# Kernel optimization log

Measured on AMD Instinct MI355X. Metric: run time of the kernel, lower is better.

The kernel has to match this reference:

```python
import jax, jax.numpy as jnp
import numpy as np

NMS_RADIUS = 0.05  # matches init_kwargs nms_radius


def setup_inputs() -> dict:
    key = jax.random.key(0)
    heatmap = jax.random.normal(key, (64, 1, 1024, 1024), dtype=jnp.float32)
    return {"heatmap": heatmap, "num_candidates": 16}


def _nms_select(coords, num_keep, radius):
    """Greedy sequential 2D NMS over score-sorted coords [k,2].
    torch.topk already returns values sorted descending, so the torch
    argsort(descending=True) is the identity permutation here."""
    k = coords.shape[0]
    # pairwise euclidean distances [k,k]
    d = jnp.linalg.norm(coords[:, None, :] - coords[None, :, :], axis=-1)

    def body(carry, i):
        mask, count = carry  # mask[j] = candidate j already selected
        too_close = jnp.any((d[i] < radius) & mask)
        accept = jnp.logical_and(~too_close, count < num_keep)
        mask = mask.at[i].set(accept)
        count = count + accept.astype(jnp.int32)
        return (mask, count), None

    (mask, _), _ = jax.lax.scan(body, (jnp.zeros(k, bool), jnp.int32(0)), jnp.arange(k))
    # compact: place selected coords (in score order) into the first num_keep slots
    pos = jnp.cumsum(mask) - 1               # output slot for each selected candidate
    slot = jnp.where(mask, pos, num_keep)    # out-of-range slot for unselected -> dropped
    out = jnp.zeros((num_keep, 2), coords.dtype).at[slot].set(coords, mode="drop")
    return out


def reference(heatmap, num_candidates):
    B, _, H, W = heatmap.shape
    flat = heatmap.reshape(B, H * W)
    k = min(num_candidates * 4, H * W)
    top_vals, top_idx = jax.lax.top_k(flat, k)   # sorted descending, like torch.topk
    ty = top_idx // W
    tx = top_idx % W
    # normalized (x, y) in [0,1], shape [B, k, 2]
    coords = jnp.stack([tx.astype(jnp.float32) / (W - 1),
                        ty.astype(jnp.float32) / (H - 1)], axis=-1)
    return jax.vmap(lambda c: _nms_select(c, num_candidates, NMS_RADIUS))(coords)
```

## Files before the change

### kernel.cpp

```cpp
#include <hip/hip_runtime.h>

#define RADIUS 0.05f
#define TH     3.0f
#define SBUF   256
#define SORTN  2048
#define TOPC   128

typedef unsigned long long u64;

__device__ __forceinline__ unsigned fkey(float f) {
  unsigned u = __float_as_uint(f);
  return (u & 0x80000000u) ? ~u : (u | 0x80000000u);
}

__global__ __launch_bounds__(256) void scan_collect(
    const float* __restrict__ hm, unsigned* __restrict__ cnt,
    u64* __restrict__ buf, int bcapblk, int elems, int chunk) {
  const int b   = blockIdx.y;
  const int g   = blockIdx.x;
  const int tid = threadIdx.x;
  const int vbase = g * chunk;
  const float4* p = (const float4*)(hm + (size_t)b * elems) + vbase;

  __shared__ u64 sbuf[SBUF];
  __shared__ unsigned sh;
  if (tid == 0) sh = 0u;
  __syncthreads();

  auto push = [&](float v, int idx) {
    if (v > TH) {
      unsigned pos = atomicAdd(&sh, 1u);
      if (pos < SBUF)
        sbuf[pos] = ((u64)(__float_as_uint(v) | 0x80000000u) << 32) | (unsigned)(~idx);
    }
  };

  int chunkMain = chunk & ~1023;
  for (int i = tid; i < chunkMain; i += 1024) {
    float4 v0 = p[i], v1 = p[i + 256], v2 = p[i + 512], v3 = p[i + 768];
    int g0 = (vbase + i) << 2, g1 = (vbase + i + 256) << 2;
    int g2 = (vbase + i + 512) << 2, g3 = (vbase + i + 768) << 2;
    push(v0.x, g0); push(v0.y, g0 + 1); push(v0.z, g0 + 2); push(v0.w, g0 + 3);
    push(v1.x, g1); push(v1.y, g1 + 1); push(v1.z, g1 + 2); push(v1.w, g1 + 3);
    push(v2.x, g2); push(v2.y, g2 + 1); push(v2.z, g2 + 2); push(v2.w, g2 + 3);
    push(v3.x, g3); push(v3.y, g3 + 1); push(v3.z, g3 + 2); push(v3.w, g3 + 3);
  }
  for (int i = chunkMain + tid; i < chunk; i += 256) {
    float4 v = p[i];
    int gg = (vbase + i) << 2;
    push(v.x, gg); push(v.y, gg + 1); push(v.z, gg + 2); push(v.w, gg + 3);
  }

  __syncthreads();
  unsigned h = sh;
  unsigned cap = (unsigned)bcapblk; if (cap > (unsigned)SBUF) cap = SBUF;
  unsigned stored = h < cap ? h : cap;
  u64* dst = buf + (size_t)(b * 16 + g) * (size_t)bcapblk;
  for (unsigned i = tid; i < stored; i += 256) dst[i] = sbuf[i];
  if (tid == 0)
    cnt[b * 16 + g] = stored | (h > stored ? 0x80000000u : 0u);
}

__global__ __launch_bounds__(256) void select_k(
    const float* __restrict__ hm, const unsigned* __restrict__ cnt,
    const u64* __restrict__ buf, int bcapblk,
    float* __restrict__ out, int W, int H, int K, int nk, int elems) {
  const int b = blockIdx.x, tid = threadIdx.x;

  __shared__ u64 s[SORTN];
  __shared__ unsigned skey[SORTN];
  __shared__ u64 top[TOPC];
  __shared__ unsigned segoff[17];
  __shared__ int s_good, s_m;
  __shared__ unsigned s_cnt;
  __shared__ float topx[64], topy[64];
  __shared__ float outbuf[128];

  if (tid == 0) {
    unsigned tot = 0; int ok = (bcapblk > 0);
    for (int g = 0; g < 16; g++) {
      unsigned cv = (bcapblk > 0) ? cnt[b * 16 + g] : 0u;
      segoff[g] = tot;
      if (cv & 0x80000000u) ok = 0;
      tot += (cv & 0x7FFFFFFFu);
    }
    segoff[16] = tot;
    s_good = ok && tot >= (unsigned)K && tot <= (unsigned)SORTN;
    s_m = 0;
  }
  __syncthreads();
  const int good = s_good;
  const unsigned c = segoff[16];

  if (good) {
    for (int g = 0; g < 16; g++) {
      unsigned off = segoff[g], len = segoff[g + 1] - off;
      const u64* src = buf + (size_t)(b * 16 + g) * (size_t)bcapblk;
      for (unsigned i = tid; i < len; i += 256) {
        u64 e = src[i];
        s[off + i] = e;
        skey[off + i] = (unsigned)(e >> 32);
      }
    }
    __syncthreads();

    unsigned lo = 0xC0400000u;
    unsigned hi = 0xFFFFFFFFu;
    while (lo < hi) {
      unsigned mid = lo + ((hi - lo) >> 1) + 1u;
      if (tid == 0) s_cnt = 0u;
      __syncthreads();
      unsigned local = 0;
      for (unsigned i = tid; i < c; i += 256) local += (skey[i] >= mid);
      #pragma unroll
      for (int o = 32; o > 0; o >>= 1) local += __shfl_xor(local, o);
      if ((tid & 63) == 0) atomicAdd(&s_cnt, local);
      __syncthreads();
      unsigned tot = s_cnt;
      if (tot >= (unsigned)K) lo = mid; else hi = mid - 1u;
      __syncthreads();
    }

    for (unsigned i = tid; i < c; i += 256) {
      if (skey[i] >= lo) {
        int p = atomicAdd(&s_m, 1);
        if (p < TOPC) top[p] = s[i];
      }
    }
    __syncthreads();
  } else {
    unsigned lo = 0u, hi = 0xFFFFFFFFu;
    const float4* p4 = (const float4*)(hm + (size_t)b * elems);
    const int nvec4 = elems >> 2;
    while (lo < hi) {
      unsigned mid = lo + ((hi - lo) >> 1) + 1u;
      if (tid == 0) s_cnt = 0u;
      __syncthreads();
      unsigned local = 0;
      for (int i = tid; i < nvec4; i += 256) {
        float4 v = p4[i];
        local += (fkey(v.x) >= mid) + (fkey(v.y) >= mid) + (fkey(v.z) >= mid) + (fkey(v.w) >= mid);
      }
      #pragma unroll
      for (int o = 32; o > 0; o >>= 1) local += __shfl_xor(local, o);
      if ((tid & 63) == 0) atomicAdd(&s_cnt, local);
      __syncthreads();
      if (s_cnt >= (unsigned)K) lo = mid; else hi = mid - 1u;
      __syncthreads();
    }
    const float* q = hm + (size_t)b * elems;
    for (int i = tid; i < elems; i += 256) {
      unsigned kk = fkey(q[i]);
      if (kk >= lo) {
        int p = atomicAdd(&s_m, 1);
        if (p < TOPC) top[p] = ((u64)kk << 32) | (unsigned)(~i);
      }
    }
    __syncthreads();
  }

  int m = s_m; if (m > TOPC) m = TOPC;
  for (int i = tid; i < TOPC; i += 256) if (i >= m) top[i] = 0ull;
  __syncthreads();
  for (int k2 = 2; k2 <= TOPC; k2 <<= 1) {
    for (int j = k2 >> 1; j > 0; j >>= 1) {
      if (tid < TOPC) {
        int ix = tid ^ j;
        if (ix > tid) {
          u64 a = top[tid], bb = top[ix];
          bool desc = ((tid & k2) == 0);
          if (desc ? (a < bb) : (a > bb)) { top[tid] = bb; top[ix] = a; }
        }
      }
      __syncthreads();
    }
  }

  const float invW = 1.0f / (float)(W - 1);
  const float invH = 1.0f / (float)(H - 1);
  if (tid < K) {
    u64 e = top[tid];
    int idx = (int)(~(unsigned)(e & 0xFFFFFFFFu));
    int ty = idx / W;
    int tx = idx - ty * W;
    topx[tid] = (float)tx * invW;
    topy[tid] = (float)ty * invH;
  }
  for (int i = tid; i < 2 * nk; i += 256) outbuf[i] = 0.0f;
  __syncthreads();

  if (tid < 64) {
    float myx = (tid < K) ? topx[tid] : 0.0f;
    float myy = (tid < K) ? topy[tid] : 0.0f;
    bool sel = false;
    int cntA = 0;
    for (int i = 0; i < K; i++) {
      float xi = __shfl(myx, i);
      float yi = __shfl(myy, i);
      float dx = myx - xi, dy = myy - yi;
      bool close = sel && (sqrtf(dx * dx + dy * dy) < RADIUS);
      u64 anym = __ballot(close);
      bool accept = (anym == 0ull) && (cntA < nk);
      if (tid == i) sel = accept;
      cntA += accept ? 1 : 0;
    }
    u64 selball = __ballot(sel);
    if (sel) {
      int slot = __popcll(selball & ((1ull << tid) - 1ull));
      if (slot < nk) { outbuf[2 * slot] = myx; outbuf[2 * slot + 1] = myy; }
    }
  }
  __syncthreads();

  float* outp = out + (size_t)b * 2 * nk;
  for (int i = tid; i < 2 * nk; i += 256) outp[i] = outbuf[i];
}

extern "C" void kernel_launch(void* const* d_in, const int* in_sizes, int n_in,
                              void* d_out, int out_size, void* d_ws, size_t ws_size,
                              hipStream_t stream) {
  const float* hm = (const float*)d_in[0];
  const int H = 1024, W = 1024;
  const int elems = H * W;
  int B = in_sizes[0] / elems;
  int nk = out_size / (B * 2);
  int K = 4 * nk;
  if (K > elems) K = elems;
  if (K > 64) K = 64;

  unsigned* cnt = (unsigned*)d_ws;
  size_t off_buf = ((size_t)B * 16 * sizeof(unsigned) + 255) & ~(size_t)255;
  u64* buf = (u64*)((char*)d_ws + off_buf);
  int bcapblk = 0;
  if (ws_size > off_buf) {
    size_t avail = ws_size - off_buf;
    long long capl = (long long)(avail / ((size_t)B * 16 * sizeof(u64)));
    bcapblk = (capl > SBUF) ? SBUF : (int)capl;
    if (bcapblk < 16) bcapblk = 0;
  }

  if (bcapblk > 0) {
    const int gx = 16;
    int chunk = (elems >> 2) / gx;
    dim3 grid(gx, B);
    scan_collect<<<grid, 256, 0, stream>>>(hm, cnt, buf, bcapblk, elems, chunk);
  }
  select_k<<<B, 256, 0, stream>>>(hm, cnt, buf, bcapblk, (float*)d_out, W, H, K, nk, elems);
}
```

Before: 400.3 us.

## Deepen nontemporal streaming loads and trim barriers in threshold search

The scan kernel now issues eight nontemporal 16-byte loads per thread per iteration instead of four regular ones, raising memory-level parallelism and bypassing cache retention for the streamed heatmap. The selection kernel splits the packed candidates into separate key and index arrays, bounds the binary search by the actual min/max key, and uses double-buffered accumulators with running bases so each search step needs one barrier instead of three. The risk is extra register pressure in the scan loop. The dominant cost is likely the bandwidth-bound scan, so gains may be small.

```diff
diff --git a/kernel.cpp b/kernel.cpp
--- a/kernel.cpp
+++ b/kernel.cpp
@@ -7,6 +7,7 @@
 #define TOPC   128
 
 typedef unsigned long long u64;
+typedef float __attribute__((ext_vector_type(4))) f4;
 
 __device__ __forceinline__ unsigned fkey(float f) {
   unsigned u = __float_as_uint(f);
@@ -20,7 +21,7 @@
   const int g   = blockIdx.x;
   const int tid = threadIdx.x;
   const int vbase = g * chunk;
-  const float4* p = (const float4*)(hm + (size_t)b * elems) + vbase;
+  const f4* p = (const f4*)(hm + (size_t)b * elems) + vbase;
 
   __shared__ u64 sbuf[SBUF];
   __shared__ unsigned sh;
@@ -35,18 +36,28 @@
     }
   };
 
-  int chunkMain = chunk & ~1023;
-  for (int i = tid; i < chunkMain; i += 1024) {
-    float4 v0 = p[i], v1 = p[i + 256], v2 = p[i + 512], v3 = p[i + 768];
-    int g0 = (vbase + i) << 2, g1 = (vbase + i + 256) << 2;
-    int g2 = (vbase + i + 512) << 2, g3 = (vbase + i + 768) << 2;
-    push(v0.x, g0); push(v0.y, g0 + 1); push(v0.z, g0 + 2); push(v0.w, g0 + 3);
-    push(v1.x, g1); push(v1.y, g1 + 1); push(v1.z, g1 + 2); push(v1.w, g1 + 3);
-    push(v2.x, g2); push(v2.y, g2 + 1); push(v2.z, g2 + 2); push(v2.w, g2 + 3);
-    push(v3.x, g3); push(v3.y, g3 + 1); push(v3.z, g3 + 2); push(v3.w, g3 + 3);
+  int chunkMain = chunk & ~2047;
+  for (int i = tid; i < chunkMain; i += 2048) {
+    f4 v0 = __builtin_nontemporal_load(p + i);
+    f4 v1 = __builtin_nontemporal_load(p + i + 256);
+    f4 v2 = __builtin_nontemporal_load(p + i + 512);
+    f4 v3 = __builtin_nontemporal_load(p + i + 768);
+    f4 v4 = __builtin_nontemporal_load(p + i + 1024);
+    f4 v5 = __builtin_nontemporal_load(p + i + 1280);
+    f4 v6 = __builtin_nontemporal_load(p + i + 1536);
+    f4 v7 = __builtin_nontemporal_load(p + i + 1792);
+    int g0 = (vbase + i) << 2;
+    push(v0.x, g0);        push(v0.y, g0 + 1);    push(v0.z, g0 + 2);    push(v0.w, g0 + 3);
+    push(v1.x, g0 + 1024); push(v1.y, g0 + 1025); push(v1.z, g0 + 1026); push(v1.w, g0 + 1027);
+    push(v2.x, g0 + 2048); push(v2.y, g0 + 2049); push(v2.z, g0 + 2050); push(v2.w, g0 + 2051);
+    push(v3.x, g0 + 3072); push(v3.y, g0 + 3073); push(v3.z, g0 + 3074); push(v3.w, g0 + 3075);
+    push(v4.x, g0 + 4096); push(v4.y, g0 + 4097); push(v4.z, g0 + 4098); push(v4.w, g0 + 4099);
+    push(v5.x, g0 + 5120); push(v5.y, g0 + 5121); push(v5.z, g0 + 5122); push(v5.w, g0 + 5123);
+    push(v6.x, g0 + 6144); push(v6.y, g0 + 6145); push(v6.z, g0 + 6146); push(v6.w, g0 + 6147);
+    push(v7.x, g0 + 7168); push(v7.y, g0 + 7169); push(v7.z, g0 + 7170); push(v7.w, g0 + 7171);
   }
   for (int i = chunkMain + tid; i < chunk; i += 256) {
-    float4 v = p[i];
+    f4 v = __builtin_nontemporal_load(p + i);
     int gg = (vbase + i) << 2;
     push(v.x, gg); push(v.y, gg + 1); push(v.z, gg + 2); push(v.w, gg + 3);
   }
@@ -67,11 +78,13 @@
     float* __restrict__ out, int W, int H, int K, int nk, int elems) {
   const int b = blockIdx.x, tid = threadIdx.x;
 
-  __shared__ u64 s[SORTN];
   __shared__ unsigned skey[SORTN];
+  __shared__ unsigned sidx[SORTN];
   __shared__ u64 top[TOPC];
   __shared__ unsigned segoff[17];
   __shared__ int s_good, s_m;
+  __shared__ unsigned s_acc[2];
+  __shared__ unsigned s_kmin, s_kmax;
   __shared__ unsigned s_cnt;
   __shared__ float topx[64], topy[64];
   __shared__ float outbuf[128];
@@ -87,44 +100,57 @@
     segoff[16] = tot;
     s_good = ok && tot >= (unsigned)K && tot <= (unsigned)SORTN;
     s_m = 0;
+    s_acc[0] = 0u; s_acc[1] = 0u;
+    s_kmin = 0xFFFFFFFFu; s_kmax = 0u;
   }
   __syncthreads();
   const int good = s_good;
   const unsigned c = segoff[16];
 
   if (good) {
+    unsigned lkmin = 0xFFFFFFFFu, lkmax = 0u;
     for (int g = 0; g < 16; g++) {
       unsigned off = segoff[g], len = segoff[g + 1] - off;
       const u64* src = buf + (size_t)(b * 16 + g) * (size_t)bcapblk;
       for (unsigned i = tid; i < len; i += 256) {
         u64 e = src[i];
-        s[off + i] = e;
-        skey[off + i] = (unsigned)(e >> 32);
-      }
-    }
+        unsigned k32 = (unsigned)(e >> 32);
+        skey[off + i] = k32;
+        sidx[off + i] = (unsigned)(e & 0xFFFFFFFFu);
+        lkmin = lkmin < k32 ? lkmin : k32;
+        lkmax = lkmax > k32 ? lkmax : k32;
+      }
+    }
+    #pragma unroll
+    for (int o = 32; o > 0; o >>= 1) {
+      unsigned a = __shfl_xor(lkmin, o); lkmin = lkmin < a ? lkmin : a;
+      unsigned bx = __shfl_xor(lkmax, o); lkmax = lkmax > bx ? lkmax : bx;
+    }
+    if ((tid & 63) == 0) { atomicMin(&s_kmin, lkmin); atomicMax(&s_kmax, lkmax); }
     __syncthreads();
 
-    unsigned lo = 0xC0400000u;
-    unsigned hi = 0xFFFFFFFFu;
+    unsigned lo = s_kmin, hi = s_kmax;
+    unsigned base0 = 0u, base1 = 0u;
+    int it = 0;
     while (lo < hi) {
       unsigned mid = lo + ((hi - lo) >> 1) + 1u;
-      if (tid == 0) s_cnt = 0u;
-      __syncthreads();
       unsigned local = 0;
       for (unsigned i = tid; i < c; i += 256) local += (skey[i] >= mid);
       #pragma unroll
       for (int o = 32; o > 0; o >>= 1) local += __shfl_xor(local, o);
-      if ((tid & 63) == 0) atomicAdd(&s_cnt, local);
-      __syncthreads();
-      unsigned tot = s_cnt;
+      if ((tid & 63) == 0) atomicAdd(&s_acc[it & 1], local);
+      __syncthreads();
+      unsigned acc = s_acc[it & 1];
+      unsigned tot = acc - ((it & 1) ? base1 : base0);
+      if (it & 1) base1 = acc; else base0 = acc;
       if (tot >= (unsigned)K) lo = mid; else hi = mid - 1u;
-      __syncthreads();
+      it++;
     }
 
     for (unsigned i = tid; i < c; i += 256) {
       if (skey[i] >= lo) {
         int p = atomicAdd(&s_m, 1);
-        if (p < TOPC) top[p] = s[i];
+        if (p < TOPC) top[p] = ((u64)skey[i] << 32) | sidx[i];
       }
     }
     __syncthreads();
```

After: 370.5 us. 7.4% less time.
